# Kernel tuning notes

Hardware: AMD Instinct MI355X
Metric: run time of the kernel (lower is better)

## Reference

```python
import jax, jax.numpy as jnp
import numpy as np

B, T, D = 32, 512, 256
F = 256  # duration_predictor_filter_size
K = 3    # kernel size, padding=1
MEL_MAX = 2304
EPS = 1e-5


def _conv1d(x, w, b):
    # x: [B, T, C_in], w: [C_out, C_in, K], 'same'-ish padding=1
    y = jax.lax.conv_general_dilated(
        x.transpose(0, 2, 1), w, window_strides=(1,), padding=[(1, 1)],
        dimension_numbers=("NCH", "OIH", "NCH"))
    return y.transpose(0, 2, 1) + b


def _layernorm(x, g, b):
    mu = jnp.mean(x, axis=-1, keepdims=True)
    var = jnp.mean(jnp.square(x - mu), axis=-1, keepdims=True)
    return (x - mu) * jax.lax.rsqrt(var + EPS) * g + b


def setup_inputs() -> dict:
    key = jax.random.key(0)
    ks = jax.random.split(key, 8)
    x = jax.random.normal(ks[0], (B, T, D), dtype=jnp.float32)
    target = jax.random.randint(ks[1], (B, T), 0, 8, dtype=jnp.int32)
    s = 0.02
    return {
        "x": x,
        "target": target,
        "mel_max_length": MEL_MAX,
        "conv1_w": jax.random.normal(ks[2], (F, D, K), dtype=jnp.float32) * s,
        "conv1_b": jnp.zeros((F,), jnp.float32),
        "ln1_g": jnp.ones((F,), jnp.float32),
        "ln1_b": jnp.zeros((F,), jnp.float32),
        "conv2_w": jax.random.normal(ks[3], (F, F, K), dtype=jnp.float32) * s,
        "conv2_b": jnp.zeros((F,), jnp.float32),
        "ln2_g": jnp.ones((F,), jnp.float32),
        "ln2_b": jnp.zeros((F,), jnp.float32),
        "lin_w": jax.random.normal(ks[4], (1, F), dtype=jnp.float32) * s,
        "lin_b": jnp.zeros((1,), jnp.float32),
    }


def reference(x, target, mel_max_length, conv1_w, conv1_b, ln1_g, ln1_b,
              conv2_w, conv2_b, ln2_g, ln2_b, lin_w, lin_b):
    # Variance_adaptor (duration predictor), eval-mode dropout = identity
    h = jax.nn.relu(_layernorm(_conv1d(x, conv1_w, conv1_b), ln1_g, ln1_b))
    h = jax.nn.relu(_layernorm(_conv1d(h, conv2_w, conv2_b), ln2_g, ln2_b))
    dur_pred = jax.nn.relu(jnp.einsum("btf,of->bto", h, lin_w) + lin_b)[..., 0]  # [B,T]

    # LR: alignment @ x, expressed as the equivalent duration-indexed gather.
    # alignment[b, t_out, j] = 1 iff cumsum(dur)[b,j-1] <= t_out < cumsum(dur)[b,j]
    cum = jnp.cumsum(target, axis=1)                    # [B, T]
    t_out = jnp.arange(mel_max_length, dtype=cum.dtype)  # [T_out]
    idx = jax.vmap(lambda c: jnp.searchsorted(c, t_out, side="right"))(cum)  # [B, T_out]
    valid = (t_out[None, :] < cum[:, -1:]).astype(x.dtype)                   # [B, T_out]
    gathered = jnp.take_along_axis(x, jnp.clip(idx, 0, T - 1)[:, :, None], axis=1)
    output = gathered * valid[:, :, None]                # zeros past total length (pad)
    return output, dur_pred
```

## Files before the change

### kernel.cpp

```cpp
#include <hip/hip_runtime.h>

typedef __attribute__((ext_vector_type(8))) short short8;
typedef __attribute__((ext_vector_type(4))) float floatx4;

typedef __attribute__((address_space(3))) unsigned int lds_u32;
typedef __attribute__((address_space(1))) const unsigned int glb_u32;

static __device__ __forceinline__ unsigned short f2bf(float f) {
    unsigned int u = __float_as_uint(f);
    return (unsigned short)((u + 0x7FFFu + ((u >> 16) & 1u)) >> 16);
}
static __device__ __forceinline__ void cp16(const ushort* g, ushort* l) {
    __builtin_amdgcn_global_load_lds((glb_u32*)g, (lds_u32*)l, 16, 0, 0);
}

__global__ __launch_bounds__(256)
void prep_kernel(const float* __restrict__ x,
                 const float* __restrict__ w1, const float* __restrict__ w2,
                 ushort* __restrict__ xb, ushort* __restrict__ h1b,
                 ushort* __restrict__ w1q, ushort* __restrict__ w2q)
{
    const int blk = blockIdx.x, tid = threadIdx.x;
    if (blk < 4112) {
        const int r = blk * 4 + (tid >> 6);
        const int c = (tid & 63) * 4;
        const int b = r / 514, tp = r % 514;
        ushort4 o;
        if (tp >= 1 && tp <= 512) {
            float4 v = *(const float4*)(x + ((size_t)(b * 512 + tp - 1) * 256 + c));
            o.x = f2bf(v.x); o.y = f2bf(v.y); o.z = f2bf(v.z); o.w = f2bf(v.w);
        } else {
            o.x = o.y = o.z = o.w = 0;
            *(ushort4*)(h1b + (size_t)r * 256 + c) = o;
        }
        *(ushort4*)(xb + (size_t)r * 256 + c) = o;
    } else {
        const bool second = blk >= 4880;
        const int e = (blk - (second ? 4880 : 4112)) * 256 + tid;
        const float* w = second ? w2 : w1;
        ushort* wq = second ? w2q : w1q;
        const int f = e / 768, j = e % 768;
        const int c = j & 255, kr = j >> 8;
        const int se = kr * 4 + (c >> 6);
        const int kk = c & 63;
        const int wg = f >> 6, ni = (f >> 4) & 3, colf = f & 15;
        const int kh = kk >> 5, qk = (kk >> 3) & 3, jj = kk & 7;
        wq[(size_t)se * 16384 + wg * 4096 + (ni * 2 + kh) * 512
           + (qk * 16 + colf) * 8 + jj] = f2bf(w[f * 768 + c * 3 + kr]);
    }
}

template<bool IS_CONV2>
__global__ __launch_bounds__(256, 3)
void conv_mfma_kernel(const ushort* __restrict__ src,
                      const ushort* __restrict__ wq,
                      const float* __restrict__ cbias,
                      const float* __restrict__ gamma, const float* __restrict__ beta,
                      const float* __restrict__ lw, const float* __restrict__ lb,
                      ushort* __restrict__ outb,
                      float* __restrict__ durp,
                      const float* __restrict__ x,
                      const int* __restrict__ target,
                      float* __restrict__ out0,
                      int gbase)
{
    __shared__ ushort As[2][2048];
    __shared__ float sum_s[4][32], sq_s[4][32], mu_s[32], rs_s[32];
    __shared__ int cum[512], ps[256], sidx[64];

    const int tid = threadIdx.x;
    const int grp = blockIdx.x / 17, rmod = blockIdx.x % 17;

    if (rmod >= 8) {
        const int bg = gbase + grp * 9 + (rmod - 8);
        const int b = bg / 36, t0o = (bg % 36) * 64;
        const int v0 = target[b * 512 + 2 * tid];
        const int v1 = target[b * 512 + 2 * tid + 1];
        ps[tid] = v0 + v1;
        __syncthreads();
        for (int off = 1; off < 256; off <<= 1) {
            int t = (tid >= off) ? ps[tid - off] : 0;
            __syncthreads();
            ps[tid] += t;
            __syncthreads();
        }
        const int excl = tid ? ps[tid - 1] : 0;
        cum[2 * tid]     = excl + v0;
        cum[2 * tid + 1] = excl + v0 + v1;
        __syncthreads();
        const int total = cum[511];
        if (tid < 64) {
            int t = t0o + tid;
            int lo = 0, hi = 512;
            while (lo < hi) {
                int mid = (lo + hi) >> 1;
                if (cum[mid] <= t) lo = mid + 1; else hi = mid;
            }
            sidx[tid] = (t < total) ? ((lo < 512) ? lo : 511) : -1;
        }
        __syncthreads();
        const float4* x4 = (const float4*)x;
        float4* o4 = (float4*)out0;
        const int lane6 = tid & 63, g4 = tid >> 6;
        #pragma unroll 4
        for (int rr = 0; rr < 16; ++rr) {
            int r = rr * 4 + g4;
            int idx = sidx[r];
            float4 v = make_float4(0.f, 0.f, 0.f, 0.f);
            if (idx >= 0) v = x4[((size_t)(b * 512 + idx)) * 64 + lane6];
            o4[((size_t)(b * 2304 + t0o + r)) * 64 + lane6] = v;
        }
        return;
    }
    const int conv_id = grp * 8 + rmod;

    const int w_ = tid >> 6, lane = tid & 63;
    const int q = lane >> 4, col = lane & 15;
    const int b  = conv_id & 31;
    const int t0 = (conv_id >> 5) << 5;
    const int rot = conv_id % 12;

    floatx4 acc[2][4] = {};
    const int arow = tid >> 3, aquad = (tid & 7) ^ (arow & 7);
    const ushort* xbb = src + (size_t)b * 514 * 256;
    const ushort* bptr = wq + (size_t)w_ * 4096 + lane * 8;

    auto se_of = [&](int s) { int v = s + rot; return v >= 12 ? v - 12 : v; };
#define STAGE_A(SE_, BUF_) do {                                                   \
        const int se_ = (SE_);                                                    \
        const int krow_ = se_ >> 2, cbo_ = (se_ & 3) << 6;                        \
        cp16(xbb + (size_t)(t0 + krow_ + arow) * 256 + cbo_ + aquad * 8,          \
             &As[BUF_][0] + w_ * 512);                                            \
    } while (0)

    STAGE_A(se_of(0), 0);
    __syncthreads();

    int cur = 0;
    #pragma unroll
    for (int s = 0; s < 12; ++s) {
        const int nb = cur ^ 1;
        if (s + 1 < 12) STAGE_A(se_of(s + 1), nb);
        const int se = se_of(s);
        short8 bf[4][2], af[2][2];
        #pragma unroll
        for (int ni = 0; ni < 4; ++ni)
            #pragma unroll
            for (int kh = 0; kh < 2; ++kh)
                bf[ni][kh] = *(const short8*)(bptr + (size_t)se * 16384 + (ni * 2 + kh) * 512);
        #pragma unroll
        for (int mi = 0; mi < 2; ++mi)
            #pragma unroll
            for (int kh = 0; kh < 2; ++kh)
                af[mi][kh] = *(const short8*)((const char*)&As[cur][0]
                    + (mi * 16 + col) * 128 + (((kh * 4 + q) ^ (col & 7)) * 16));
        #pragma unroll
        for (int kh = 0; kh < 2; ++kh)
            #pragma unroll
            for (int mi = 0; mi < 2; ++mi)
                #pragma unroll
                for (int ni = 0; ni < 4; ++ni)
                    acc[mi][ni] = __builtin_amdgcn_mfma_f32_16x16x32_bf16(
                        af[mi][kh], bf[ni][kh], acc[mi][ni], 0, 0, 0);
        __syncthreads();
        cur = nb;
    }
#undef STAGE_A

    const int base_c = w_ * 64;
    float cb4[4], gm4[4], bt4[4];
    #pragma unroll
    for (int ni = 0; ni < 4; ++ni) {
        cb4[ni] = cbias[base_c + ni * 16 + col];
        gm4[ni] = gamma[base_c + ni * 16 + col];
        bt4[ni] = beta [base_c + ni * 16 + col];
    }
    float rsum[2][4] = {}, rsq[2][4] = {};
    #pragma unroll
    for (int mi = 0; mi < 2; ++mi)
        #pragma unroll
        for (int ni = 0; ni < 4; ++ni)
            #pragma unroll
            for (int r = 0; r < 4; ++r) {
                float v = acc[mi][ni][r] + cb4[ni];
                acc[mi][ni][r] = v;
                rsum[mi][r] += v;
                rsq [mi][r] += v * v;
            }
    #pragma unroll
    for (int mi = 0; mi < 2; ++mi)
        #pragma unroll
        for (int r = 0; r < 4; ++r) {
            float s = rsum[mi][r], ss = rsq[mi][r];
            #pragma unroll
            for (int d = 8; d > 0; d >>= 1) {
                s  += __shfl_down(s,  d, 16);
                ss += __shfl_down(ss, d, 16);
            }
            if (col == 0) {
                sum_s[w_][mi * 16 + q * 4 + r] = s;
                sq_s [w_][mi * 16 + q * 4 + r] = ss;
            }
        }
    __syncthreads();
    if (tid < 32) {
        float s  = sum_s[0][tid] + sum_s[1][tid] + sum_s[2][tid] + sum_s[3][tid];
        float ss = sq_s [0][tid] + sq_s [1][tid] + sq_s [2][tid] + sq_s [3][tid];
        float mu = s * (1.f / 256.f);
        mu_s[tid] = mu;
        rs_s[tid] = rsqrtf(ss * (1.f / 256.f) - mu * mu + 1e-5f);
    }
    __syncthreads();

    if (!IS_CONV2) {
        #pragma unroll
        for (int mi = 0; mi < 2; ++mi)
            #pragma unroll
            for (int ni = 0; ni < 4; ++ni)
                #pragma unroll
                for (int r = 0; r < 4; ++r) {
                    int row = mi * 16 + q * 4 + r;
                    float v = (acc[mi][ni][r] - mu_s[row]) * rs_s[row] * gm4[ni] + bt4[ni];
                    outb[((size_t)b * 514 + t0 + row + 1) * 256 + base_c + ni * 16 + col]
                        = f2bf(fmaxf(v, 0.f));
                }
    } else {
        float lw4[4];
        #pragma unroll
        for (int ni = 0; ni < 4; ++ni) lw4[ni] = lw[base_c + ni * 16 + col];
        float dsum[2][4] = {};
        #pragma unroll
        for (int mi = 0; mi < 2; ++mi)
            #pragma unroll
            for (int ni = 0; ni < 4; ++ni)
                #pragma unroll
                for (int r = 0; r < 4; ++r) {
                    int row = mi * 16 + q * 4 + r;
                    float v = (acc[mi][ni][r] - mu_s[row]) * rs_s[row] * gm4[ni] + bt4[ni];
                    dsum[mi][r] += fmaxf(v, 0.f) * lw4[ni];
                }
        #pragma unroll
        for (int mi = 0; mi < 2; ++mi)
            #pragma unroll
            for (int r = 0; r < 4; ++r) {
                float s = dsum[mi][r];
                #pragma unroll
                for (int d = 8; d > 0; d >>= 1) s += __shfl_down(s, d, 16);
                if (col == 0) sum_s[w_][mi * 16 + q * 4 + r] = s;
            }
        __syncthreads();
        if (tid < 32)
            durp[b * 512 + t0 + tid] = fmaxf(sum_s[0][tid] + sum_s[1][tid]
                                           + sum_s[2][tid] + sum_s[3][tid] + lb[0], 0.f);
    }
}

extern "C" void kernel_launch(void* const* d_in, const int* in_sizes, int n_in,
                              void* d_out, int out_size, void* d_ws, size_t ws_size,
                              hipStream_t stream) {
    const float* x      = (const float*)d_in[0];
    const int*   target = (const int*)  d_in[1];
    const float* c1w = (const float*)d_in[3];
    const float* c1b = (const float*)d_in[4];
    const float* g1  = (const float*)d_in[5];
    const float* b1  = (const float*)d_in[6];
    const float* c2w = (const float*)d_in[7];
    const float* c2b = (const float*)d_in[8];
    const float* g2  = (const float*)d_in[9];
    const float* b2  = (const float*)d_in[10];
    const float* lw  = (const float*)d_in[11];
    const float* lb  = (const float*)d_in[12];

    const size_t PADEL = (size_t)32 * 514 * 256;
    ushort* xb   = (ushort*)d_ws;
    ushort* h1b  = xb + PADEL;
    ushort* w1q  = h1b + PADEL;
    ushort* w2q  = w1q + 196608;

    float* out0 = (float*)d_out;
    float* durp = out0 + (size_t)32 * 2304 * 256;

    prep_kernel<<<5648, 256, 0, stream>>>(x, c1w, c2w, xb, h1b, w1q, w2q);
    conv_mfma_kernel<false><<<1088, 256, 0, stream>>>(
        xb, w1q, c1b, g1, b1, nullptr, nullptr, h1b, nullptr,
        x, target, out0, 0);
    conv_mfma_kernel<true><<<1088, 256, 0, stream>>>(
        h1b, w2q, c2b, g2, b2, lw, lb, nullptr, durp,
        x, target, out0, 576);
}
```

Baseline: 152.0 us.

## Load full input slab once per conv block; precompute cumsum in prep kernel

The conv kernel now stages the whole 34-row activation slab into LDS in one pass, replacing the per-step double-buffered staging that had a barrier on each of the 12 K-steps. Source rows are stored pre-swizzled (an XOR on 16-byte chunks) by the prep and conv1 epilogue, so LDS reads avoid bank conflicts without extra index work at load time. The duration cumsum is computed once per batch in extra prep blocks rather than redone by every gather block, and gather outputs use nontemporal stores. The trade-off is more LDS per block (about 18KB), which may reduce occupancy, and the full slab load must finish before any MFMA can start.

```diff
diff --git a/kernel.cpp b/kernel.cpp
--- a/kernel.cpp
+++ b/kernel.cpp
@@ -2,6 +2,7 @@
 
 typedef __attribute__((ext_vector_type(8))) short short8;
 typedef __attribute__((ext_vector_type(4))) float floatx4;
+typedef __attribute__((ext_vector_type(4))) float f4v;
 
 typedef __attribute__((address_space(3))) unsigned int lds_u32;
 typedef __attribute__((address_space(1))) const unsigned int glb_u32;
@@ -14,27 +15,31 @@
     __builtin_amdgcn_global_load_lds((glb_u32*)g, (lds_u32*)l, 16, 0, 0);
 }
 
+
 __global__ __launch_bounds__(256)
-void prep_kernel(const float* __restrict__ x,
+void prep_kernel(const float* __restrict__ x, const int* __restrict__ target,
                  const float* __restrict__ w1, const float* __restrict__ w2,
                  ushort* __restrict__ xb, ushort* __restrict__ h1b,
-                 ushort* __restrict__ w1q, ushort* __restrict__ w2q)
+                 ushort* __restrict__ w1q, ushort* __restrict__ w2q,
+                 int* __restrict__ cumg)
 {
+    __shared__ int ps[256];
     const int blk = blockIdx.x, tid = threadIdx.x;
     if (blk < 4112) {
         const int r = blk * 4 + (tid >> 6);
         const int c = (tid & 63) * 4;
         const int b = r / 514, tp = r % 514;
+        const int e2 = ((((c >> 3) ^ (tp & 7)) << 3) | (c & 7));
         ushort4 o;
         if (tp >= 1 && tp <= 512) {
             float4 v = *(const float4*)(x + ((size_t)(b * 512 + tp - 1) * 256 + c));
             o.x = f2bf(v.x); o.y = f2bf(v.y); o.z = f2bf(v.z); o.w = f2bf(v.w);
         } else {
             o.x = o.y = o.z = o.w = 0;
-            *(ushort4*)(h1b + (size_t)r * 256 + c) = o;
-        }
-        *(ushort4*)(xb + (size_t)r * 256 + c) = o;
-    } else {
+            *(ushort4*)(h1b + (size_t)r * 256 + e2) = o;
+        }
+        *(ushort4*)(xb + (size_t)r * 256 + e2) = o;
+    } else if (blk < 5648) {
         const bool second = blk >= 4880;
         const int e = (blk - (second ? 4880 : 4112)) * 256 + tid;
         const float* w = second ? w2 : w1;
@@ -47,6 +52,21 @@
         const int kh = kk >> 5, qk = (kk >> 3) & 3, jj = kk & 7;
         wq[(size_t)se * 16384 + wg * 4096 + (ni * 2 + kh) * 512
            + (qk * 16 + colf) * 8 + jj] = f2bf(w[f * 768 + c * 3 + kr]);
+    } else {
+        const int b = blk - 5648;
+        const int v0 = target[b * 512 + 2 * tid];
+        const int v1 = target[b * 512 + 2 * tid + 1];
+        ps[tid] = v0 + v1;
+        __syncthreads();
+        for (int off = 1; off < 256; off <<= 1) {
+            int t = (tid >= off) ? ps[tid - off] : 0;
+            __syncthreads();
+            ps[tid] += t;
+            __syncthreads();
+        }
+        const int excl = tid ? ps[tid - 1] : 0;
+        cumg[b * 512 + 2 * tid]     = excl + v0;
+        cumg[b * 512 + 2 * tid + 1] = excl + v0 + v1;
     }
 }
 
@@ -60,13 +80,13 @@
                       ushort* __restrict__ outb,
                       float* __restrict__ durp,
                       const float* __restrict__ x,
-                      const int* __restrict__ target,
+                      const int* __restrict__ cumg,
                       float* __restrict__ out0,
                       int gbase)
 {
-    __shared__ ushort As[2][2048];
+    __shared__ ushort slab[36 * 256];
     __shared__ float sum_s[4][32], sq_s[4][32], mu_s[32], rs_s[32];
-    __shared__ int cum[512], ps[256], sidx[64];
+    __shared__ int cum_s[512], sidx[64];
 
     const int tid = threadIdx.x;
     const int grp = blockIdx.x / 17, rmod = blockIdx.x % 17;
@@ -74,41 +94,30 @@
     if (rmod >= 8) {
         const int bg = gbase + grp * 9 + (rmod - 8);
         const int b = bg / 36, t0o = (bg % 36) * 64;
-        const int v0 = target[b * 512 + 2 * tid];
-        const int v1 = target[b * 512 + 2 * tid + 1];
-        ps[tid] = v0 + v1;
+        cum_s[tid]       = cumg[b * 512 + tid];
+        cum_s[tid + 256] = cumg[b * 512 + 256 + tid];
         __syncthreads();
-        for (int off = 1; off < 256; off <<= 1) {
-            int t = (tid >= off) ? ps[tid - off] : 0;
-            __syncthreads();
-            ps[tid] += t;
-            __syncthreads();
-        }
-        const int excl = tid ? ps[tid - 1] : 0;
-        cum[2 * tid]     = excl + v0;
-        cum[2 * tid + 1] = excl + v0 + v1;
-        __syncthreads();
-        const int total = cum[511];
+        const int total = cum_s[511];
         if (tid < 64) {
             int t = t0o + tid;
             int lo = 0, hi = 512;
             while (lo < hi) {
                 int mid = (lo + hi) >> 1;
-                if (cum[mid] <= t) lo = mid + 1; else hi = mid;
+                if (cum_s[mid] <= t) lo = mid + 1; else hi = mid;
             }
             sidx[tid] = (t < total) ? ((lo < 512) ? lo : 511) : -1;
         }
         __syncthreads();
-        const float4* x4 = (const float4*)x;
-        float4* o4 = (float4*)out0;
+        const f4v* x4 = (const f4v*)x;
+        f4v* o4 = (f4v*)out0;
         const int lane6 = tid & 63, g4 = tid >> 6;
         #pragma unroll 4
         for (int rr = 0; rr < 16; ++rr) {
             int r = rr * 4 + g4;
             int idx = sidx[r];
-            float4 v = make_float4(0.f, 0.f, 0.f, 0.f);
+            f4v v = {0.f, 0.f, 0.f, 0.f};
             if (idx >= 0) v = x4[((size_t)(b * 512 + idx)) * 64 + lane6];
-            o4[((size_t)(b * 2304 + t0o + r)) * 64 + lane6] = v;
+            __builtin_nontemporal_store(v, &o4[((size_t)(b * 2304 + t0o + r)) * 64 + lane6]);
         }
         return;
     }
@@ -120,28 +129,26 @@
     const int t0 = (conv_id >> 5) << 5;
     const int rot = conv_id % 12;
 
+    const ushort* xbb = src + (size_t)b * 514 * 256;
+    #pragma unroll
+    for (int r = 0; r < 4; ++r) {
+        const int i = r * 8 + w_ * 2 + (lane >> 5);
+        cp16(xbb + (size_t)(t0 + i) * 256 + (lane & 31) * 8,
+             slab + r * 2048 + w_ * 512);
+    }
+    if (w_ < 2) {
+        const int i = 32 + w_ * 2 + (lane >> 5);
+        cp16(xbb + (size_t)(t0 + i) * 256 + (lane & 31) * 8,
+             slab + 8192 + w_ * 512);
+    }
+    __syncthreads();
+
     floatx4 acc[2][4] = {};
-    const int arow = tid >> 3, aquad = (tid & 7) ^ (arow & 7);
-    const ushort* xbb = src + (size_t)b * 514 * 256;
     const ushort* bptr = wq + (size_t)w_ * 4096 + lane * 8;
-
-    auto se_of = [&](int s) { int v = s + rot; return v >= 12 ? v - 12 : v; };
-#define STAGE_A(SE_, BUF_) do {                                                   \
-        const int se_ = (SE_);                                                    \
-        const int krow_ = se_ >> 2, cbo_ = (se_ & 3) << 6;                        \
-        cp16(xbb + (size_t)(t0 + krow_ + arow) * 256 + cbo_ + aquad * 8,          \
-             &As[BUF_][0] + w_ * 512);                                            \
-    } while (0)
-
-    STAGE_A(se_of(0), 0);
-    __syncthreads();
-
-    int cur = 0;
     #pragma unroll
     for (int s = 0; s < 12; ++s) {
-        const int nb = cur ^ 1;
-        if (s + 1 < 12) STAGE_A(se_of(s + 1), nb);
-        const int se = se_of(s);
+        int se = s + rot; if (se >= 12) se -= 12;
+        const int krow = se >> 2, cb8 = (se & 3) << 3;
         short8 bf[4][2], af[2][2];
         #pragma unroll
         for (int ni = 0; ni < 4; ++ni)
@@ -149,11 +156,14 @@
             for (int kh = 0; kh < 2; ++kh)
                 bf[ni][kh] = *(const short8*)(bptr + (size_t)se * 16384 + (ni * 2 + kh) * 512);
         #pragma unroll
-        for (int mi = 0; mi < 2; ++mi)
-            #pragma unroll
-            for (int kh = 0; kh < 2; ++kh)
-                af[mi][kh] = *(const short8*)((const char*)&As[cur][0]
-                    + (mi * 16 + col) * 128 + (((kh * 4 + q) ^ (col & 7)) * 16));
+        for (int mi = 0; mi < 2; ++mi) {
+            #pragma unroll
+            for (int kh = 0; kh < 2; ++kh) {
+                const int i = krow + mi * 16 + col;
+                const int ch = cb8 + kh * 4 + q;
+                af[mi][kh] = *(const short8*)(slab + i * 256 + ((ch ^ (i & 7)) << 3));
+            }
+        }
         #pragma unroll
         for (int kh = 0; kh < 2; ++kh)
             #pragma unroll
@@ -162,10 +172,7 @@
                 for (int ni = 0; ni < 4; ++ni)
                     acc[mi][ni] = __builtin_amdgcn_mfma_f32_16x16x32_bf16(
                         af[mi][kh], bf[ni][kh], acc[mi][ni], 0, 0, 0);
-        __syncthreads();
-        cur = nb;
-    }
-#undef STAGE_A
+    }
 
     const int base_c = w_ * 64;
     float cb4[4], gm4[4], bt4[4];
@@ -221,8 +228,10 @@
                 for (int r = 0; r < 4; ++r) {
                     int row = mi * 16 + q * 4 + r;
                     float v = (acc[mi][ni][r] - mu_s[row]) * rs_s[row] * gm4[ni] + bt4[ni];
-                    outb[((size_t)b * 514 + t0 + row + 1) * 256 + base_c + ni * 16 + col]
-                        = f2bf(fmaxf(v, 0.f));
+                    const int tp = t0 + row + 1;
+                    const int cc = base_c + ni * 16 + col;
+                    const int e2 = ((((cc >> 3) ^ (tp & 7)) << 3) | (cc & 7));
+                    outb[((size_t)b * 514 + tp) * 256 + e2] = f2bf(fmaxf(v, 0.f));
                 }
     } else {
         float lw4[4];
@@ -276,15 +285,16 @@
     ushort* h1b  = xb + PADEL;
     ushort* w1q  = h1b + PADEL;
     ushort* w2q  = w1q + 196608;
+    int*    cumg = (int*)(w2q + 196608);
 
     float* out0 = (float*)d_out;
     float* durp = out0 + (size_t)32 * 2304 * 256;
 
-    prep_kernel<<<5648, 256, 0, stream>>>(x, c1w, c2w, xb, h1b, w1q, w2q);
+    prep_kernel<<<5680, 256, 0, stream>>>(x, target, c1w, c2w, xb, h1b, w1q, w2q, cumg);
     conv_mfma_kernel<false><<<1088, 256, 0, stream>>>(
         xb, w1q, c1b, g1, b1, nullptr, nullptr, h1b, nullptr,
-        x, target, out0, 0);
+        x, cumg, out0, 0);
     conv_mfma_kernel<true><<<1088, 256, 0, stream>>>(
         h1b, w2q, c2b, g2, b2, lw, lb, nullptr, durp,
-        x, target, out0, 576);
-}
+        x, cumg, out0, 576);
+}
```

Result: no change. 150.7 us (-0.8%).
